# Kernel optimization log

Hardware: AMD Instinct MI355X
Metric: run time of the kernel (lower is better)

The kernel has to match this reference:

```python
import jax, jax.numpy as jnp
import numpy as np

N_NODES = 50000
N_EDGES = 500000
HIDDEN = 64
HEADS = 8
VOCAB = 40000
N_GRAPHS = 512


def setup_inputs() -> dict:
    key = jax.random.key(0)
    ks = jax.random.split(key, 16)
    s = 0.05  # keep attention logits in a sane range
    emb = jax.random.normal(ks[0], (VOCAB + 1, HIDDEN), jnp.float32) * s
    emb = emb.at[0].set(0.0)  # padding_idx=0
    return {
        'x': jax.random.randint(ks[1], (N_NODES,), 0, VOCAB + 1),
        'edge_index': jax.random.randint(ks[2], (2, N_EDGES), 0, N_NODES),
        'batch': jnp.sort(jax.random.randint(ks[3], (N_NODES,), 0, N_GRAPHS)),
        'emb': emb,
        'W1': jax.random.normal(ks[4], (HIDDEN, HEADS * HIDDEN), jnp.float32) * s,
        'a_src1': jax.random.normal(ks[5], (HEADS, HIDDEN), jnp.float32) * s,
        'a_dst1': jax.random.normal(ks[6], (HEADS, HIDDEN), jnp.float32) * s,
        'b1': jax.random.normal(ks[7], (HEADS * HIDDEN,), jnp.float32) * s,
        'W2': jax.random.normal(ks[8], (HEADS * HIDDEN, HIDDEN), jnp.float32) * s,
        'a_src2': jax.random.normal(ks[9], (1, HIDDEN), jnp.float32) * s,
        'a_dst2': jax.random.normal(ks[10], (1, HIDDEN), jnp.float32) * s,
        'b2': jax.random.normal(ks[11], (HIDDEN,), jnp.float32) * s,
        'Wp': jax.random.normal(ks[12], (HIDDEN, VOCAB), jnp.float32) * s,
        'bp': jax.random.normal(ks[13], (VOCAB,), jnp.float32) * s,
    }


def _gat_conv(h, src, dst, W, a_src, a_dst, b, heads, out_c, concat):
    # PyG GATConv (eval mode, self-loops already appended by caller).
    n = h.shape[0]
    hp = (h @ W).reshape(n, heads, out_c)              # [N, H, C]
    s_src = jnp.einsum('nhc,hc->nh', hp, a_src)        # per-node src score
    s_dst = jnp.einsum('nhc,hc->nh', hp, a_dst)        # per-node dst score
    logits = jax.nn.leaky_relu(s_src[src] + s_dst[dst], negative_slope=0.2)  # [E, H]
    # segment softmax over destination-node neighborhoods
    m = jax.ops.segment_max(logits, dst, num_segments=n)
    m = jnp.where(jnp.isfinite(m), m, 0.0)
    e = jnp.exp(logits - m[dst])
    denom = jax.ops.segment_sum(e, dst, num_segments=n)
    alpha = e / (denom[dst] + 1e-16)                   # [E, H]
    msgs = hp[src] * alpha[:, :, None]                 # [E, H, C]
    out = jax.ops.segment_sum(msgs, dst, num_segments=n)
    out = out.reshape(n, heads * out_c) if concat else out.mean(axis=1)
    return out + b


def reference(x, edge_index, batch, emb, W1, a_src1, a_dst1, b1, W2, a_src2, a_dst2, b2, Wp, bp):
    n = x.shape[0]
    loop = jnp.arange(n)
    src = jnp.concatenate([edge_index[0], loop])  # add_self_loops=True
    dst = jnp.concatenate([edge_index[1], loop])
    h = emb[x]                                     # embedding lookup [N, 64]
    h = jax.nn.elu(_gat_conv(h, src, dst, W1, a_src1, a_dst1, b1, HEADS, HIDDEN, True))
    h = _gat_conv(h, src, dst, W2, a_src2, a_dst2, b2, 1, HIDDEN, False)
    pooled = jax.ops.segment_sum(h, batch, num_segments=N_GRAPHS)  # global_add_pool
    return pooled @ Wp + bp
```

## Files before the change

### kernel.cpp

```cpp
#include <hip/hip_runtime.h>
#include <hip/hip_bf16.h>
#include <hip/hip_fp16.h>

#define N_NODESC 50000
#define N_EDGESC 500000
#define E_TOT    (N_EDGESC + N_NODESC)
#define HID      64
#define HEADS_C  8
#define F1       (HEADS_C * HID)
#define VOCAB_C  40000
#define N_GR     512
#define SCAN_B   196

typedef __attribute__((ext_vector_type(8))) short bf16x8;
typedef __attribute__((ext_vector_type(4))) float f32x4;
typedef __attribute__((ext_vector_type(8))) _Float16 half8;

__device__ __forceinline__ float lrelu(float x) { return x > 0.f ? x : 0.2f * x; }
__device__ __forceinline__ float bf2f(unsigned short u) {
  return __uint_as_float(((unsigned int)u) << 16);
}
__device__ __forceinline__ unsigned short f2bf(float f) {
  unsigned int u = __float_as_uint(f);
  unsigned int r = (u + 0x7fffu + ((u >> 16) & 1u)) >> 16;
  return (unsigned short)r;
}
__device__ __forceinline__ unsigned short f2h(float f) {
  __half h = __float2half(f);
  union { __half h; unsigned short u; } c; c.h = h; return c.u;
}
__device__ __forceinline__ __half2 as_h2(unsigned int v) {
  union { unsigned int u; __half2 h; } c; c.u = v; return c.h;
}
__device__ __forceinline__ unsigned int h2u(__half2 h) {
  union { __half2 h; unsigned int u; } c; c.h = h; return c.u;
}

__global__ void k_zero(int* __restrict__ deg, float* __restrict__ pooled) {
  int i = blockIdx.x * 256 + threadIdx.x;
  if (i < N_NODESC) deg[i] = 0;
  if (i < N_GR * HID) pooled[i] = 0.f;
}

__global__ void k_deg(const int* __restrict__ ei, int* __restrict__ deg,
                      int* __restrict__ eslot) {
  int e = blockIdx.x * blockDim.x + threadIdx.x;
  if (e >= E_TOT) return;
  int dst = (e < N_EDGESC) ? ei[N_EDGESC + e] : (e - N_EDGESC);
  eslot[e] = atomicAdd(&deg[dst], 1);
}

__global__ __launch_bounds__(256) void k_scan1(const int* __restrict__ deg,
                                               int* __restrict__ rowtmp,
                                               int* __restrict__ partials) {
  __shared__ int sh[256];
  int b = blockIdx.x, t = threadIdx.x, i = b * 256 + t;
  int d = (i < N_NODESC) ? deg[i] : 0;
  sh[t] = d;
  __syncthreads();
  for (int o = 1; o < 256; o <<= 1) {
    int v = (t >= o) ? sh[t - o] : 0;
    __syncthreads();
    sh[t] += v;
    __syncthreads();
  }
  if (i < N_NODESC) rowtmp[i] = sh[t];
  if (t == 255) partials[b] = sh[255];
}

__global__ __launch_bounds__(256) void k_scan3(const int* __restrict__ deg,
                                               const int* __restrict__ rowtmp,
                                               const int* __restrict__ partials,
                                               int* __restrict__ rowstart) {
  __shared__ int wsum[4];
  int b = blockIdx.x, t = threadIdx.x;
  int acc = 0;
  for (int i = t; i < b; i += 256) acc += partials[i];
#pragma unroll
  for (int o = 32; o; o >>= 1) acc += __shfl_xor(acc, o);
  if ((t & 63) == 0) wsum[t >> 6] = acc;
  __syncthreads();
  int base = wsum[0] + wsum[1] + wsum[2] + wsum[3];
  int i = b * 256 + t;
  if (i < N_NODESC) rowstart[i] = base + rowtmp[i] - deg[i];
  if (i == N_NODESC - 1) rowstart[N_NODESC] = base + rowtmp[i];
}

__global__ void k_scatter(const int* __restrict__ ei, const int* __restrict__ rowstart,
                          const int* __restrict__ eslot, int* __restrict__ esrc) {
  int e = blockIdx.x * blockDim.x + threadIdx.x;
  if (e >= E_TOT) return;
  int src, dst;
  if (e < N_EDGESC) { src = ei[e]; dst = ei[N_EDGESC + e]; }
  else { src = dst = e - N_EDGESC; }
  esrc[rowstart[dst] + eslot[e]] = src;
}

__global__ __launch_bounds__(512) void k_prepwconv(const float* __restrict__ W1,
                                                   const float* __restrict__ as1,
                                                   const float* __restrict__ ad1,
                                                   const float* __restrict__ W2,
                                                   const float* __restrict__ as2,
                                                   const float* __restrict__ ad2,
                                                   const float* __restrict__ Wp,
                                                   float* __restrict__ w2sv,
                                                   float* __restrict__ w2dv,
                                                   unsigned short* __restrict__ waB,
                                                   unsigned short* __restrict__ w1bT,
                                                   unsigned short* __restrict__ w2bT,
                                                   unsigned short* __restrict__ wpT) {
  __shared__ float ws[64][65];
  int b = blockIdx.x, t = threadIdx.x;
  if (b < 64) {
    int g = b * 512 + t;
    int c = g >> 6, k = g & 63;
    w1bT[g] = f2bf(W1[(size_t)k * F1 + c]);
  } else if (b < 128) {
    int idx = (b - 64) * 512 + t;
    int c = idx >> 9, k = idx & 511;
    w2bT[idx] = f2bf(W2[(size_t)k * HID + c]);
  } else if (b == 128) {
    int k = t >> 3, h = t & 7;
    float ss = 0.f, dd = 0.f;
    for (int c = 0; c < 64; ++c) {
      float w = W1[k * F1 + h * 64 + c];
      ss += w * as1[h * 64 + c];
      dd += w * ad1[h * 64 + c];
    }
    waB[h * 64 + k] = f2bf(ss);
    waB[(8 + h) * 64 + k] = f2bf(dd);
    float s2 = 0.f, d2 = 0.f;
    for (int c = 0; c < 64; ++c) {
      float w = W2[t * 64 + c];
      s2 += w * as2[c];
      d2 += w * ad2[c];
    }
    w2sv[t] = s2;
    w2dv[t] = d2;
  } else {
    int v0 = (b - 129) * 64;
#pragma unroll
    for (int rep = 0; rep < 8; ++rep) {
      int idx = rep * 512 + t;
      int k = idx >> 6, v = idx & 63;
      ws[k][v] = Wp[(size_t)k * VOCAB_C + v0 + v];
    }
    __syncthreads();
#pragma unroll
    for (int rep = 0; rep < 8; ++rep) {
      int idx = rep * 512 + t;
      int v = idx >> 6, k = idx & 63;
      wpT[(size_t)(v0 + v) * 64 + k] = f2bf(ws[k][v]);
    }
  }
}

__global__ __launch_bounds__(256) void k_embed(const int* __restrict__ x,
                                               const float* __restrict__ emb,
                                               const unsigned short* __restrict__ waB,
                                               unsigned short* __restrict__ hf,
                                               float* __restrict__ s1s,
                                               float* __restrict__ s1d) {
  int t = threadIdx.x;
  int w = t >> 6, lane = t & 63;
  int lrow = lane & 15, lq = lane >> 4;
  int n0 = blockIdx.x * 64 + w * 16;
  if (n0 >= N_NODESC) return;
  int node = n0 + lrow;
  const float* er = emb + (size_t)x[node] * 64;
  float4 f0 = *reinterpret_cast<const float4*>(er + lq * 8);
  float4 f1 = *reinterpret_cast<const float4*>(er + lq * 8 + 4);
  float4 f2 = *reinterpret_cast<const float4*>(er + 32 + lq * 8);
  float4 f3 = *reinterpret_cast<const float4*>(er + 32 + lq * 8 + 4);
  bf16x8 a0, a1;
  a0[0] = (short)f2bf(f0.x); a0[1] = (short)f2bf(f0.y);
  a0[2] = (short)f2bf(f0.z); a0[3] = (short)f2bf(f0.w);
  a0[4] = (short)f2bf(f1.x); a0[5] = (short)f2bf(f1.y);
  a0[6] = (short)f2bf(f1.z); a0[7] = (short)f2bf(f1.w);
  a1[0] = (short)f2bf(f2.x); a1[1] = (short)f2bf(f2.y);
  a1[2] = (short)f2bf(f2.z); a1[3] = (short)f2bf(f2.w);
  a1[4] = (short)f2bf(f3.x); a1[5] = (short)f2bf(f3.y);
  a1[6] = (short)f2bf(f3.z); a1[7] = (short)f2bf(f3.w);
  half8 h0, h1;
  h0[0] = (_Float16)f0.x; h0[1] = (_Float16)f0.y;
  h0[2] = (_Float16)f0.z; h0[3] = (_Float16)f0.w;
  h0[4] = (_Float16)f1.x; h0[5] = (_Float16)f1.y;
  h0[6] = (_Float16)f1.z; h0[7] = (_Float16)f1.w;
  h1[0] = (_Float16)f2.x; h1[1] = (_Float16)f2.y;
  h1[2] = (_Float16)f2.z; h1[3] = (_Float16)f2.w;
  h1[4] = (_Float16)f3.x; h1[5] = (_Float16)f3.y;
  h1[6] = (_Float16)f3.z; h1[7] = (_Float16)f3.w;
  *reinterpret_cast<half8*>(&hf[(size_t)node * 64 + lq * 8]) = h0;
  *reinterpret_cast<half8*>(&hf[(size_t)node * 64 + 32 + lq * 8]) = h1;
  const bf16x8* brow = reinterpret_cast<const bf16x8*>(waB + lrow * 64 + lq * 8);
  f32x4 acc = {};
  acc = __builtin_amdgcn_mfma_f32_16x16x32_bf16(a0, brow[0], acc, 0, 0, 0);
  acc = __builtin_amdgcn_mfma_f32_16x16x32_bf16(a1, brow[4], acc, 0, 0, 0);
  float* dst = (lrow < 8) ? s1s : s1d;
  int h = lrow & 7;
#pragma unroll
  for (int r = 0; r < 4; ++r)
    dst[(size_t)(n0 + lq * 4 + r) * 8 + h] = acc[r];
}

__global__ __launch_bounds__(256) void k_agg1(const int* __restrict__ rowstart,
                                              const int* __restrict__ esrc,
                                              const unsigned short* __restrict__ hf,
                                              const float* __restrict__ s1s,
                                              const float* __restrict__ s1d,
                                              unsigned short* __restrict__ agg8) {
  int n = blockIdx.x * 4 + (threadIdx.x >> 6);
  int L = threadIdx.x & 63;
  int eh = L >> 3;
  int hh = L & 7;
  int myh = L >> 3;
  const int fc = (L & 7) * 8;
  int r0 = rowstart[n], dg = rowstart[n + 1] - r0;
  float sdst = s1d[n * 8 + hh];
  __half2 ac0 = __float2half2_rn(0.f), ac1 = ac0, ac2 = ac0, ac3 = ac0;
  float dsum = 0.f;
  for (int base = 0; base < dg; base += 8) {
    int i = base + eh;
    float p = 0.f;
    int s = 0;
    if (i < dg) {
      s = esrc[r0 + i];
      p = __expf(lrelu(s1s[s * 8 + hh] + sdst));
    }
    dsum += p;
    int cnt = min(8, dg - base);
    if (cnt == 8) {
      int sjs[8];
#pragma unroll
      for (int j = 0; j < 8; ++j) sjs[j] = __shfl(s, j << 3);
      uint4 us[8];
#pragma unroll
      for (int j = 0; j < 8; ++j)
        us[j] = *reinterpret_cast<const uint4*>(&hf[(size_t)sjs[j] * 64 + fc]);
#pragma unroll
      for (int j = 0; j < 8; ++j) {
        __half2 p2 = __float2half2_rn(__shfl(p, (j << 3) | myh));
        ac0 = __hfma2(as_h2(us[j].x), p2, ac0);
        ac1 = __hfma2(as_h2(us[j].y), p2, ac1);
        ac2 = __hfma2(as_h2(us[j].z), p2, ac2);
        ac3 = __hfma2(as_h2(us[j].w), p2, ac3);
      }
    } else {
      for (int j = 0; j < cnt; ++j) {
        float pj = __shfl(p, (j << 3) | myh);
        int sj = __shfl(s, j << 3);
        uint4 u = *reinterpret_cast<const uint4*>(&hf[(size_t)sj * 64 + fc]);
        __half2 p2 = __float2half2_rn(pj);
        ac0 = __hfma2(as_h2(u.x), p2, ac0);
        ac1 = __hfma2(as_h2(u.y), p2, ac1);
        ac2 = __hfma2(as_h2(u.z), p2, ac2);
        ac3 = __hfma2(as_h2(u.w), p2, ac3);
      }
    }
  }
  dsum += __shfl_xor(dsum, 8);
  dsum += __shfl_xor(dsum, 16);
  dsum += __shfl_xor(dsum, 32);
  float inv = 1.f / (__shfl(dsum, myh) + 1e-16f);
  float2 v0 = __half22float2(ac0);
  float2 v1 = __half22float2(ac1);
  float2 v2 = __half22float2(ac2);
  float2 v3 = __half22float2(ac3);
  uint4 ov;
  ov.x = (unsigned int)f2bf(v0.x * inv) | ((unsigned int)f2bf(v0.y * inv) << 16);
  ov.y = (unsigned int)f2bf(v1.x * inv) | ((unsigned int)f2bf(v1.y * inv) << 16);
  ov.z = (unsigned int)f2bf(v2.x * inv) | ((unsigned int)f2bf(v2.y * inv) << 16);
  ov.w = (unsigned int)f2bf(v3.x * inv) | ((unsigned int)f2bf(v3.y * inv) << 16);
  *reinterpret_cast<uint4*>(&agg8[(size_t)n * F1 + L * 8]) = ov;
}

__global__ __launch_bounds__(256) void k_hgemm(const unsigned short* __restrict__ agg8,
                                               const unsigned short* __restrict__ w1bT,
                                               const float* __restrict__ b1,
                                               unsigned short* __restrict__ h1b) {
  __shared__ unsigned short Ts[16][520];
  __shared__ float bs[512];
  int t = threadIdx.x;
  int n0 = blockIdx.x * 16;
  bs[t] = b1[t]; bs[t + 256] = b1[t + 256];
  int w = t >> 6, lane = t & 63;
  int lrow = lane & 15, lq = lane >> 4;
  const unsigned short* arow = agg8 + (size_t)(n0 + lrow) * F1;
  int h0 = 2 * w;
  bf16x8 a00 = *reinterpret_cast<const bf16x8*>(arow + h0 * 64 + lq * 8);
  bf16x8 a01 = *reinterpret_cast<const bf16x8*>(arow + h0 * 64 + 32 + lq * 8);
  bf16x8 a10 = *reinterpret_cast<const bf16x8*>(arow + (h0 + 1) * 64 + lq * 8);
  bf16x8 a11 = *reinterpret_cast<const bf16x8*>(arow + (h0 + 1) * 64 + 32 + lq * 8);
  int c0 = w * 128;
  f32x4 acc[8] = {};
#pragma unroll
  for (int ct = 0; ct < 8; ++ct) {
    int col = c0 + ct * 16 + lrow;
    const bf16x8* brow = reinterpret_cast<const bf16x8*>(w1bT + (size_t)col * 64 + lq * 8);
    if (ct < 4) {
      acc[ct] = __builtin_amdgcn_mfma_f32_16x16x32_bf16(a00, brow[0], acc[ct], 0, 0, 0);
      acc[ct] = __builtin_amdgcn_mfma_f32_16x16x32_bf16(a01, brow[4], acc[ct], 0, 0, 0);
    } else {
      acc[ct] = __builtin_amdgcn_mfma_f32_16x16x32_bf16(a10, brow[0], acc[ct], 0, 0, 0);
      acc[ct] = __builtin_amdgcn_mfma_f32_16x16x32_bf16(a11, brow[4], acc[ct], 0, 0, 0);
    }
  }
  __syncthreads();
#pragma unroll
  for (int ct = 0; ct < 8; ++ct) {
    int col = c0 + ct * 16 + lrow;
#pragma unroll
    for (int r = 0; r < 4; ++r) {
      float v = acc[ct][r] + bs[col];
      v = v > 0.f ? v : (__expf(v) - 1.f);
      Ts[lq * 4 + r][col] = f2bf(v);
    }
  }
  __syncthreads();
  for (int i = t; i < 1024; i += 256) {
    int r = i >> 6, c16 = i & 63;
    reinterpret_cast<uint4*>(&h1b[(size_t)(n0 + r) * F1])[c16] =
        *reinterpret_cast<const uint4*>(&Ts[r][c16 * 8]);
  }
}

__global__ __launch_bounds__(256) void k_gemm2(const unsigned short* __restrict__ h1b,
                                               const unsigned short* __restrict__ w2bT,
                                               const float* __restrict__ w2sv,
                                               const float* __restrict__ w2dv,
                                               unsigned short* __restrict__ hp2h,
                                               float* __restrict__ s2s,
                                               float* __restrict__ s2d) {
  __shared__ float wsv[512], wdv[512];
  int t = threadIdx.x;
  for (int i = t; i < 512; i += 256) { wsv[i] = w2sv[i]; wdv[i] = w2dv[i]; }
  __syncthreads();
  int w = t >> 6, lane = t & 63;
  int lrow = lane & 15, lq = lane >> 4;
  int nb = blockIdx.x * 64 + w * 16;
  if (nb >= N_NODESC) return;
  f32x4 acc[4] = {};
  float ssp = 0.f, ddp = 0.f;
  const unsigned short* arowp = h1b + (size_t)(nb + lrow) * F1;
#pragma unroll 4
  for (int kq = 0; kq < 16; ++kq) {
    int kbase = kq * 32 + lq * 8;
    bf16x8 a = *reinterpret_cast<const bf16x8*>(arowp + kbase);
#pragma unroll
    for (int i = 0; i < 8; ++i) {
      float f = bf2f((unsigned short)a[i]);
      ssp += f * wsv[kbase + i];
      ddp += f * wdv[kbase + i];
    }
#pragma unroll
    for (int ct = 0; ct < 4; ++ct) {
      bf16x8 b = *reinterpret_cast<const bf16x8*>(w2bT + (size_t)(ct * 16 + lrow) * F1 + kbase);
      acc[ct] = __builtin_amdgcn_mfma_f32_16x16x32_bf16(a, b, acc[ct], 0, 0, 0);
    }
  }
  ssp += __shfl_xor(ssp, 16); ssp += __shfl_xor(ssp, 32);
  ddp += __shfl_xor(ddp, 16); ddp += __shfl_xor(ddp, 32);
  if (lane < 16) { s2s[nb + lane] = ssp; s2d[nb + lane] = ddp; }
#pragma unroll
  for (int ct = 0; ct < 4; ++ct) {
    int col = ct * 16 + lrow;
#pragma unroll
    for (int r = 0; r < 4; ++r)
      hp2h[(size_t)(nb + lq * 4 + r) * HID + col] = f2h(acc[ct][r]);
  }
}

__global__ __launch_bounds__(256) void k_agg2(const int* __restrict__ rowstart,
                                              const int* __restrict__ esrc,
                                              const unsigned short* __restrict__ hp2h,
                                              const float* __restrict__ s2s,
                                              const float* __restrict__ s2d,
                                              const float* __restrict__ b2,
                                              const int* __restrict__ batch,
                                              float* __restrict__ pooled) {
  int n = blockIdx.x * 4 + (threadIdx.x >> 6);
  int lane = threadIdx.x & 63;
  int half = lane >> 5;
  int fl = lane & 31;
  int r0 = rowstart[n], dg = rowstart[n + 1] - r0;
  float sdst = s2d[n];
  __half2 ac = __float2half2_rn(0.f);
  float dsum = 0.f;
  for (int base = 0; base < dg; base += 32) {
    int i = base + fl;
    float p = 0.f;
    int s = 0;
    if (i < dg) {
      s = esrc[r0 + i];
      p = __expf(lrelu(s2s[s] + sdst));
    }
    dsum += p;
    int cnt = min(32, dg - base);
    if (cnt == 32) {
      int sjs[16];
#pragma unroll
      for (int jj = 0; jj < 16; ++jj) sjs[jj] = __shfl(s, 2 * jj + half, 32);
      unsigned int us[16];
#pragma unroll
      for (int jj = 0; jj < 16; ++jj)
        us[jj] = *reinterpret_cast<const unsigned int*>(&hp2h[(size_t)sjs[jj] * 64 + fl * 2]);
#pragma unroll
      for (int jj = 0; jj < 16; ++jj) {
        float pj = __shfl(p, 2 * jj + half, 32);
        ac = __hfma2(as_h2(us[jj]), __float2half2_rn(pj), ac);
      }
    } else {
      for (int j = 0; j < cnt; j += 2) {
        int jj = j + half;
        float pj = __shfl(p, jj, 32);
        int sj = __shfl(s, jj, 32);
        unsigned int hv = *reinterpret_cast<const unsigned int*>(&hp2h[(size_t)sj * 64 + fl * 2]);
        ac = __hfma2(as_h2(hv), __float2half2_rn(pj), ac);
      }
    }
  }
#pragma unroll
  for (int o = 1; o < 32; o <<= 1) dsum += __shfl_xor(dsum, o);
  float inv = 1.f / (dsum + 1e-16f);
  unsigned int other = __shfl_xor(h2u(ac), 32);
  ac = __hadd2(ac, as_h2(other));
  float2 fv = __half22float2(ac);
  int f = 2 * fl + half;
  float o = (half ? fv.y : fv.x) * inv + b2[f];
  atomicAdd(&pooled[batch[n] * 64 + f], o);
}

__global__ __launch_bounds__(256) void k_final(const float* __restrict__ pooled,
                                               const unsigned short* __restrict__ wpT,
                                               const float* __restrict__ bp,
                                               float* __restrict__ out) {
  __shared__ unsigned short As[16][72];
  __shared__ float Cs[16][324];
  int t = threadIdx.x;
  int g0 = blockIdx.y * 16;
  int vb = blockIdx.x * 320;
  {
    int g = t >> 4, k4 = (t & 15) * 4;
    float4 pv = *reinterpret_cast<const float4*>(&pooled[(size_t)(g0 + g) * 64 + k4]);
    ushort4 u;
    u.x = f2bf(pv.x); u.y = f2bf(pv.y); u.z = f2bf(pv.z); u.w = f2bf(pv.w);
    *reinterpret_cast<ushort4*>(&As[g][k4]) = u;
  }
  __syncthreads();
  int w = t >> 6, lane = t & 63;
  int lrow = lane & 15, lq = lane >> 4;
  bf16x8 a0 = *reinterpret_cast<const bf16x8*>(&As[lrow][lq * 8]);
  bf16x8 a1 = *reinterpret_cast<const bf16x8*>(&As[lrow][32 + lq * 8]);
#pragma unroll
  for (int ct = 0; ct < 5; ++ct) {
    int cloc = (w * 5 + ct) * 16 + lrow;
    const bf16x8* brow = reinterpret_cast<const bf16x8*>(wpT + (size_t)(vb + cloc) * 64 + lq * 8);
    f32x4 acc = {};
    acc = __builtin_amdgcn_mfma_f32_16x16x32_bf16(a0, brow[0], acc, 0, 0, 0);
    acc = __builtin_amdgcn_mfma_f32_16x16x32_bf16(a1, brow[4], acc, 0, 0, 0);
#pragma unroll
    for (int r = 0; r < 4; ++r) Cs[lq * 4 + r][cloc] = acc[r];
  }
  __syncthreads();
  for (int i = t; i < 1280; i += 256) {
    int r = i / 80, c = i % 80;
    float4 cv = *reinterpret_cast<const float4*>(&Cs[r][c * 4]);
    float4 bv = *reinterpret_cast<const float4*>(&bp[vb + c * 4]);
    cv.x += bv.x; cv.y += bv.y; cv.z += bv.z; cv.w += bv.w;
    *reinterpret_cast<float4*>(&out[(size_t)(g0 + r) * VOCAB_C + vb + c * 4]) = cv;
  }
}

extern "C" void kernel_launch(void* const* d_in, const int* in_sizes, int n_in,
                              void* d_out, int out_size, void* d_ws, size_t ws_size,
                              hipStream_t stream) {
  const int*   x     = (const int*)d_in[0];
  const int*   ei    = (const int*)d_in[1];
  const int*   batch = (const int*)d_in[2];
  const float* emb   = (const float*)d_in[3];
  const float* W1    = (const float*)d_in[4];
  const float* as1   = (const float*)d_in[5];
  const float* ad1   = (const float*)d_in[6];
  const float* b1    = (const float*)d_in[7];
  const float* W2    = (const float*)d_in[8];
  const float* as2   = (const float*)d_in[9];
  const float* ad2   = (const float*)d_in[10];
  const float* b2    = (const float*)d_in[11];
  const float* Wp    = (const float*)d_in[12];
  const float* bp    = (const float*)d_in[13];
  float* out = (float*)d_out;

  char* ws = (char*)d_ws;
  size_t off = 0;
#define WS_ALLOC(T, name, bytes) T name = (T)(ws + off); off += (((size_t)(bytes)) + 255) & ~(size_t)255;
  WS_ALLOC(unsigned short*, hf,   (size_t)N_NODESC * HID * 2)
  WS_ALLOC(unsigned short*, agg8, (size_t)N_NODESC * F1 * 2)
  WS_ALLOC(unsigned short*, h1b,  (size_t)N_NODESC * F1 * 2)
  WS_ALLOC(unsigned short*, hp2h, (size_t)N_NODESC * HID * 2)
  WS_ALLOC(unsigned short*, w1bT, 512 * 64 * 2)
  WS_ALLOC(unsigned short*, w2bT, 64 * 512 * 2)
  WS_ALLOC(unsigned short*, wpT,  (size_t)VOCAB_C * HID * 2)
  WS_ALLOC(unsigned short*, waB,  16 * 64 * 2)
  WS_ALLOC(float*, s1s,  (size_t)N_NODESC * HEADS_C * 4)
  WS_ALLOC(float*, s1d,  (size_t)N_NODESC * HEADS_C * 4)
  WS_ALLOC(float*, s2s,  (size_t)N_NODESC * 4)
  WS_ALLOC(float*, s2d,  (size_t)N_NODESC * 4)
  WS_ALLOC(float*, pooled, (size_t)N_GR * HID * 4)
  WS_ALLOC(float*, w2sv, 512 * 4)
  WS_ALLOC(float*, w2dv, 512 * 4)
  WS_ALLOC(int*,   deg,      (size_t)N_NODESC * 4)
  WS_ALLOC(int*,   rowstart, (size_t)(N_NODESC + 1) * 4)
  WS_ALLOC(int*,   rowtmp,   (size_t)N_NODESC * 4)
  WS_ALLOC(int*,   partials, 256 * 4)
  WS_ALLOC(int*,   eslot,    (size_t)E_TOT * 4)
  WS_ALLOC(int*,   esrc,     (size_t)E_TOT * 4)
#undef WS_ALLOC
  (void)ws_size; (void)in_sizes; (void)n_in; (void)out_size;

  int ethreads = 256, eblocks = (E_TOT + 255) / 256;
  k_zero<<<SCAN_B, 256, 0, stream>>>(deg, pooled);
  k_deg<<<eblocks, ethreads, 0, stream>>>(ei, deg, eslot);
  k_scan1<<<SCAN_B, 256, 0, stream>>>(deg, rowtmp, partials);
  k_scan3<<<SCAN_B, 256, 0, stream>>>(deg, rowtmp, partials, rowstart);
  k_scatter<<<eblocks, ethreads, 0, stream>>>(ei, rowstart, eslot, esrc);
  k_prepwconv<<<129 + VOCAB_C / 64, 512, 0, stream>>>(
      W1, as1, ad1, W2, as2, ad2, Wp,
      w2sv, w2dv, waB, w1bT, w2bT, wpT);

  k_embed<<<(N_NODESC + 63) / 64, 256, 0, stream>>>(x, emb, waB, hf, s1s, s1d);
  k_agg1<<<N_NODESC / 4, 256, 0, stream>>>(rowstart, esrc, hf, s1s, s1d, agg8);
  k_hgemm<<<N_NODESC / 16, 256, 0, stream>>>(agg8, w1bT, b1, h1b);

  k_gemm2<<<(N_NODESC + 63) / 64, 256, 0, stream>>>(h1b, w2bT, w2sv, w2dv, hp2h, s2s, s2d);
  k_agg2<<<N_NODESC / 4, 256, 0, stream>>>(rowstart, esrc, hp2h, s2s, s2d, b2, batch, pooled);

  k_final<<<dim3(VOCAB_C / 320, N_GR / 16), 256, 0, stream>>>(pooled, wpT, bp, out);
}
```

Measured before the change: 252.9 us.

## Fuse layer-1 head GEMM with layer-2 projection GEMM through shared memory

```diff
diff --git a/kernel.cpp b/kernel.cpp
--- a/kernel.cpp
+++ b/kernel.cpp
@@ -274,15 +274,23 @@
   *reinterpret_cast<uint4*>(&agg8[(size_t)n * F1 + L * 8]) = ov;
 }
 
-__global__ __launch_bounds__(256) void k_hgemm(const unsigned short* __restrict__ agg8,
-                                               const unsigned short* __restrict__ w1bT,
-                                               const float* __restrict__ b1,
-                                               unsigned short* __restrict__ h1b) {
+__global__ __launch_bounds__(256) void k_fused12(const unsigned short* __restrict__ agg8,
+                                                 const unsigned short* __restrict__ w1bT,
+                                                 const float* __restrict__ b1,
+                                                 const unsigned short* __restrict__ w2bT,
+                                                 const float* __restrict__ w2sv,
+                                                 const float* __restrict__ w2dv,
+                                                 unsigned short* __restrict__ hp2h,
+                                                 float* __restrict__ s2s,
+                                                 float* __restrict__ s2d) {
   __shared__ unsigned short Ts[16][520];
-  __shared__ float bs[512];
+  __shared__ float bs[512], wsv[512], wdv[512];
+  __shared__ float sredS[4][16], sredD[4][16];
   int t = threadIdx.x;
   int n0 = blockIdx.x * 16;
   bs[t] = b1[t]; bs[t + 256] = b1[t + 256];
+  wsv[t] = w2sv[t]; wsv[t + 256] = w2sv[t + 256];
+  wdv[t] = w2dv[t]; wdv[t + 256] = w2dv[t + 256];
   int w = t >> 6, lane = t & 63;
   int lrow = lane & 15, lq = lane >> 4;
   const unsigned short* arow = agg8 + (size_t)(n0 + lrow) * F1;
@@ -306,6 +314,7 @@
     }
   }
   __syncthreads();
+  float ssp[4] = {}, ddp[4] = {};
 #pragma unroll
   for (int ct = 0; ct < 8; ++ct) {
     int col = c0 + ct * 16 + lrow;
@@ -314,60 +323,38 @@
       float v = acc[ct][r] + bs[col];
       v = v > 0.f ? v : (__expf(v) - 1.f);
       Ts[lq * 4 + r][col] = f2bf(v);
-    }
+      ssp[r] += v * wsv[col];
+      ddp[r] += v * wdv[col];
+    }
+  }
+#pragma unroll
+  for (int r = 0; r < 4; ++r) {
+#pragma unroll
+    for (int o = 1; o < 16; o <<= 1) {
+      ssp[r] += __shfl_xor(ssp[r], o);
+      ddp[r] += __shfl_xor(ddp[r], o);
+    }
+  }
+  if (lrow == 0) {
+#pragma unroll
+    for (int r = 0; r < 4; ++r) { sredS[w][lq * 4 + r] = ssp[r]; sredD[w][lq * 4 + r] = ddp[r]; }
   }
   __syncthreads();
-  for (int i = t; i < 1024; i += 256) {
-    int r = i >> 6, c16 = i & 63;
-    reinterpret_cast<uint4*>(&h1b[(size_t)(n0 + r) * F1])[c16] =
-        *reinterpret_cast<const uint4*>(&Ts[r][c16 * 8]);
-  }
-}
-
-__global__ __launch_bounds__(256) void k_gemm2(const unsigned short* __restrict__ h1b,
-                                               const unsigned short* __restrict__ w2bT,
-                                               const float* __restrict__ w2sv,
-                                               const float* __restrict__ w2dv,
-                                               unsigned short* __restrict__ hp2h,
-                                               float* __restrict__ s2s,
-                                               float* __restrict__ s2d) {
-  __shared__ float wsv[512], wdv[512];
-  int t = threadIdx.x;
-  for (int i = t; i < 512; i += 256) { wsv[i] = w2sv[i]; wdv[i] = w2dv[i]; }
-  __syncthreads();
-  int w = t >> 6, lane = t & 63;
-  int lrow = lane & 15, lq = lane >> 4;
-  int nb = blockIdx.x * 64 + w * 16;
-  if (nb >= N_NODESC) return;
-  f32x4 acc[4] = {};
-  float ssp = 0.f, ddp = 0.f;
-  const unsigned short* arowp = h1b + (size_t)(nb + lrow) * F1;
+  f32x4 acc2 = {};
 #pragma unroll 4
   for (int kq = 0; kq < 16; ++kq) {
     int kbase = kq * 32 + lq * 8;
-    bf16x8 a = *reinterpret_cast<const bf16x8*>(arowp + kbase);
-#pragma unroll
-    for (int i = 0; i < 8; ++i) {
-      float f = bf2f((unsigned short)a[i]);
-      ssp += f * wsv[kbase + i];
-      ddp += f * wdv[kbase + i];
-    }
-#pragma unroll
-    for (int ct = 0; ct < 4; ++ct) {
-      bf16x8 b = *reinterpret_cast<const bf16x8*>(w2bT + (size_t)(ct * 16 + lrow) * F1 + kbase);
-      acc[ct] = __builtin_amdgcn_mfma_f32_16x16x32_bf16(a, b, acc[ct], 0, 0, 0);
-    }
-  }
-  ssp += __shfl_xor(ssp, 16); ssp += __shfl_xor(ssp, 32);
-  ddp += __shfl_xor(ddp, 16); ddp += __shfl_xor(ddp, 32);
-  if (lane < 16) { s2s[nb + lane] = ssp; s2d[nb + lane] = ddp; }
-#pragma unroll
-  for (int ct = 0; ct < 4; ++ct) {
-    int col = ct * 16 + lrow;
-#pragma unroll
-    for (int r = 0; r < 4; ++r)
-      hp2h[(size_t)(nb + lq * 4 + r) * HID + col] = f2h(acc[ct][r]);
-  }
+    bf16x8 a = *reinterpret_cast<const bf16x8*>(&Ts[lrow][kbase]);
+    bf16x8 b = *reinterpret_cast<const bf16x8*>(w2bT + (size_t)(w * 16 + lrow) * F1 + kbase);
+    acc2 = __builtin_amdgcn_mfma_f32_16x16x32_bf16(a, b, acc2, 0, 0, 0);
+  }
+  if (t < 16) {
+    s2s[n0 + t] = sredS[0][t] + sredS[1][t] + sredS[2][t] + sredS[3][t];
+    s2d[n0 + t] = sredD[0][t] + sredD[1][t] + sredD[2][t] + sredD[3][t];
+  }
+#pragma unroll
+  for (int r = 0; r < 4; ++r)
+    hp2h[(size_t)(n0 + lq * 4 + r) * HID + w * 16 + lrow] = f2h(acc2[r]);
 }
 
 __global__ __launch_bounds__(256) void k_agg2(const int* __restrict__ rowstart,
@@ -495,7 +482,6 @@
 #define WS_ALLOC(T, name, bytes) T name = (T)(ws + off); off += (((size_t)(bytes)) + 255) & ~(size_t)255;
   WS_ALLOC(unsigned short*, hf,   (size_t)N_NODESC * HID * 2)
   WS_ALLOC(unsigned short*, agg8, (size_t)N_NODESC * F1 * 2)
-  WS_ALLOC(unsigned short*, h1b,  (size_t)N_NODESC * F1 * 2)
   WS_ALLOC(unsigned short*, hp2h, (size_t)N_NODESC * HID * 2)
   WS_ALLOC(unsigned short*, w1bT, 512 * 64 * 2)
   WS_ALLOC(unsigned short*, w2bT, 64 * 512 * 2)
@@ -529,9 +515,8 @@
 
   k_embed<<<(N_NODESC + 63) / 64, 256, 0, stream>>>(x, emb, waB, hf, s1s, s1d);
   k_agg1<<<N_NODESC / 4, 256, 0, stream>>>(rowstart, esrc, hf, s1s, s1d, agg8);
-  k_hgemm<<<N_NODESC / 16, 256, 0, stream>>>(agg8, w1bT, b1, h1b);
-
-  k_gemm2<<<(N_NODESC + 63) / 64, 256, 0, stream>>>(h1b, w2bT, w2sv, w2dv, hp2h, s2s, s2d);
+  k_fused12<<<N_NODESC / 16, 256, 0, stream>>>(agg8, w1bT, b1, w2bT, w2sv, w2dv,
+                                               hp2h, s2s, s2d);
   k_agg2<<<N_NODESC / 4, 256, 0, stream>>>(rowstart, esrc, hp2h, s2s, s2d, b2, batch, pooled);
 
   k_final<<<dim3(VOCAB_C / 320, N_GR / 16), 256, 0, stream>>>(pooled, wpT, bp, out);
```

New measurement: 234.6 us, median of 2. -7.2%, faster.
